# Kernel optimization log

Hardware: AMD Instinct MI355X
Metric: run time of the kernel (lower is better)

The kernel has to match this reference:

```python
import jax, jax.numpy as jnp
import numpy as np

IN_F = 256
LAYERS = [256, 256, 256, 256]   # layer_sizeList
DIMS = [IN_F] + LAYERS          # per-layer (in, out) = (DIMS[i], DIMS[i+1])
NUM_L = len(LAYERS)             # 4 dynamic layers (3 hidden + final identity)
CASE_IN = 64
CASE_H = 256
W_SIZE = IN_F * LAYERS[0]       # 65536, uniform across layers here
C, N = 64, 2048


def setup_inputs() -> dict:
    key = jax.random.key(0)
    k = jax.random.split(key, 8)
    x = jax.random.normal(k[0], (N, IN_F), jnp.float32)
    o = jax.random.normal(k[1], (C, CASE_IN), jnp.float32)
    # caseNN hidden layer (Linear + SiLU)
    Wc = jax.random.normal(k[2], (CASE_IN, CASE_H), jnp.float32) / np.sqrt(CASE_IN).astype(np.float32)
    bc = jnp.zeros((CASE_H,), jnp.float32)
    # final heads (identity activation): one weight head + one bias head per domain layer
    head_scale = np.float32(1.0 / (np.sqrt(CASE_H) * np.sqrt(IN_F)))
    Ww = jax.random.normal(k[3], (NUM_L, CASE_H, W_SIZE), jnp.float32) * head_scale
    bw = jnp.zeros((NUM_L, W_SIZE), jnp.float32)
    Wb = jax.random.normal(k[4], (NUM_L, CASE_H, LAYERS[0]), jnp.float32) * head_scale
    bb = jnp.zeros((NUM_L, LAYERS[0]), jnp.float32)
    return {"x": x, "o": o, "Wc": Wc, "bc": bc, "Ww": Ww, "bw": bw, "Wb": Wb, "bb": bb}


def reference(x, o, Wc, bc, Ww, bw, Wb, bb):
    # ---- caseNN (hypernetwork): generate per-case weights/biases ----
    h = jax.nn.silu(o @ Wc + bc)                     # [C, H]
    w = jnp.einsum('ch,lhd->lcd', h, Ww) + bw[:, None, :]   # [L, C, in*out]
    b = jnp.einsum('ch,lhd->lcd', h, Wb) + bb[:, None, :]   # [L, C, out]
    c = o.shape[0]

    # ---- domain net: per-case dynamic FC layers with skip connections ----
    # layer 0: broadcast shared x over cases
    W0 = w[0].reshape(c, DIMS[0], DIMS[1])
    y = jax.nn.silu(jnp.einsum('ni,cio->cno', x, W0) + b[0][:, None, :])  # [C, N, 256]
    x_skip = y  # skip_connections and i==0
    for i in range(1, NUM_L - 1):
        Wi = w[i].reshape(c, DIMS[i], DIMS[i + 1])
        y2 = jax.nn.silu(jnp.einsum('cni,cio->cno', y, Wi) + b[i][:, None, :])
        if i % 2 == 0:
            y2, x_skip = y2 + x_skip, y2
        y = y2
    # final layer: identity activation
    Wf = w[NUM_L - 1].reshape(c, DIMS[NUM_L - 1], DIMS[NUM_L])
    out = jnp.einsum('cni,cio->cno', y, Wf) + b[NUM_L - 1][:, None, :]
    return out.reshape(-1, out.shape[-1])  # [C*N, out]
```

## Files before the change

### kernel.cpp

```cpp
#include <hip/hip_runtime.h>


typedef __bf16 bf16;
typedef __bf16 bf16x4 __attribute__((ext_vector_type(4)));
typedef __bf16 bf16x8 __attribute__((ext_vector_type(8)));
typedef _Float16 f16;
typedef _Float16 f16x8 __attribute__((ext_vector_type(8)));
typedef float  f32x4  __attribute__((ext_vector_type(4)));
typedef unsigned short u16x8 __attribute__((ext_vector_type(8)));

#define AS1 __attribute__((address_space(1)))
#define AS3 __attribute__((address_space(3)))

__device__ __forceinline__ void gl2lds16(const void* g, void* l) {
  __builtin_amdgcn_global_load_lds((const AS1 unsigned int*)g,
                                   (AS3 unsigned int*)l, 16, 0, 0);
}

__device__ __forceinline__ float silu_f(float v) {
  return v / (1.0f + __expf(-v));
}

__global__ void k_hyper(const float* __restrict__ o, const float* __restrict__ Wc,
                        const float* __restrict__ bc, float* __restrict__ ht,
                        f16* __restrict__ hb16) {
  __shared__ float os[64];
  int c = blockIdx.x;
  int j = threadIdx.x;
  if (j < 64) os[j] = o[c * 64 + j];
  __syncthreads();
  float a = bc[j];
#pragma unroll
  for (int i = 0; i < 64; ++i) a = fmaf(os[i], Wc[i * 256 + j], a);
  float h = silu_f(a);
  ht[j * 64 + c] = h;
  hb16[c * 256 + j] = (f16)h;
}

__global__ void k_xcast(const float* __restrict__ x, bf16* __restrict__ xb) {
  int i = (blockIdx.x * 256 + threadIdx.x) * 4;
  float4 v = *(const float4*)(x + i);
  bf16x4 r = { (bf16)v.x, (bf16)v.y, (bf16)v.z, (bf16)v.w };
  *(bf16x4*)(xb + i) = r;
}

__global__ __launch_bounds__(512, 1) void k_genw(
    const float* __restrict__ Ww, const float* __restrict__ bw,
    const f16* __restrict__ hb16, bf16* __restrict__ wnat) {
  __shared__ __attribute__((aligned(16))) char Hs[32768];
  __shared__ __attribute__((aligned(16))) char Wslot[3][32768];
  int l = blockIdx.x >> 8;
  int d0 = (blockIdx.x & 255) * 256;
  const float* Wwl = Ww + (size_t)l * 16777216;
  int tid = threadIdx.x, lane = tid & 63, wid = tid >> 6;

  for (int q = tid; q < 2048; q += 512) {
    int c = q >> 5, g = q & 31;
    f16x8 v = *(const f16x8*)(hb16 + c * 256 + g * 8);
    *(f16x8*)(Hs + c * 512 + ((g ^ (c & 7)) << 4)) = v;
  }
  __syncthreads();

  auto STAGE = [&](int s, int t) {
#pragma unroll
    for (int ii = 0; ii < 4; ++ii) {
      int row = wid * 4 + ii;
      gl2lds16(Wwl + (size_t)(t * 32 + row) * 65536 + d0 + lane * 4,
               &Wslot[s][row * 1024]);
    }
  };

  f32x4 acc[4][2] = {};
  STAGE(0, 0);
  STAGE(1, 1);
#pragma unroll
  for (int kk = 0; kk < 8; ++kk) {
    if (kk < 6) STAGE((kk + 2) % 3, kk + 2);
    if (kk < 6)       asm volatile("s_waitcnt vmcnt(8)" ::: "memory");
    else if (kk == 6) asm volatile("s_waitcnt vmcnt(4)" ::: "memory");
    else              asm volatile("s_waitcnt vmcnt(0)" ::: "memory");
    __builtin_amdgcn_s_barrier();
    __builtin_amdgcn_sched_barrier(0);

    f16x8 af[4];
    int kc = kk * 4 + (lane >> 4);
#pragma unroll
    for (int mf = 0; mf < 4; ++mf) {
      int c = mf * 16 + (lane & 15);
      af[mf] = *(const f16x8*)(Hs + c * 512 + ((kc ^ (c & 7)) << 4));
    }
    const float* Ws = (const float*)&Wslot[kk % 3][0];
    f16x8 bfrag[2];
#pragma unroll
    for (int nf = 0; nf < 2; ++nf) {
      int n = wid * 32 + nf * 16 + (lane & 15);
#pragma unroll
      for (int j = 0; j < 8; ++j)
        bfrag[nf][j] = (f16)Ws[((lane >> 4) * 8 + j) * 256 + n];
    }
    asm volatile("s_waitcnt lgkmcnt(0)" ::: "memory");
    __builtin_amdgcn_sched_barrier(0);
    __builtin_amdgcn_s_barrier();
#pragma unroll
    for (int mf = 0; mf < 4; ++mf)
#pragma unroll
      for (int nf = 0; nf < 2; ++nf)
        acc[mf][nf] = __builtin_amdgcn_mfma_f32_16x16x32_f16(
            af[mf], bfrag[nf], acc[mf][nf], 0, 0, 0);
  }

#pragma unroll
  for (int nf = 0; nf < 2; ++nf) {
    int d = d0 + wid * 32 + nf * 16 + (lane & 15);
    float bv = bw[(size_t)l * 65536 + d];
#pragma unroll
    for (int mf = 0; mf < 4; ++mf) {
      int cb = mf * 16 + (lane >> 4) * 4;
#pragma unroll
      for (int r = 0; r < 4; ++r)
        wnat[(size_t)(l * 64 + cb + r) * 65536 + d] = (bf16)(acc[mf][nf][r] + bv);
    }
  }
}

__global__ void k_genb(const float* __restrict__ Wb, const float* __restrict__ bb,
                       const float* __restrict__ ht, float* __restrict__ bias) {
  __shared__ float red[4][256];
  int l = blockIdx.x >> 6;
  int c = blockIdx.x & 63;
  int q = threadIdx.x >> 8;
  int oo = threadIdx.x & 255;
  const float* wp = Wb + (size_t)l * 65536 + oo;
  float a = 0.f;
#pragma unroll 4
  for (int hh = q * 64; hh < q * 64 + 64; ++hh)
    a = fmaf(ht[hh * 64 + c], wp[hh * 256], a);
  red[q][oo] = a;
  __syncthreads();
  if (q == 0)
    bias[(size_t)(l * 64 + c) * 256 + oo] =
        red[0][oo] + red[1][oo] + red[2][oo] + red[3][oo] + bb[l * 256 + oo];
}

__global__ void k_tw(const unsigned short* __restrict__ w,
                     unsigned short* __restrict__ wt) {
  __shared__ __attribute__((aligned(16))) unsigned short T[64][64];
  int b = blockIdx.x;
  int lc = b >> 4, tile = b & 15;
  int i0 = (tile >> 2) << 6, o0 = (tile & 3) << 6;
  const unsigned short* src = w + (size_t)lc * 65536;
  unsigned short* dst = wt + (size_t)lc * 65536;
  int t = threadIdx.x;
  for (int q = t; q < 512; q += 256) {
    int r = q >> 3, cc = q & 7;
    u16x8 v = *(const u16x8*)(src + (size_t)(i0 + r) * 256 + o0 + cc * 8);
    *(u16x8*)&T[r][(cc ^ ((r >> 3) & 7)) * 8] = v;
  }
  __syncthreads();
  for (int q = t; q < 512; q += 256) {
    int r = q >> 3, cc = q & 7;
    u16x8 v;
#pragma unroll
    for (int e = 0; e < 8; ++e) {
      int il = cc * 8 + e;
      v[e] = T[il][((((r >> 3) ^ (il >> 3)) & 7) << 3) + (r & 7)];
    }
    *(u16x8*)(dst + (size_t)(o0 + r) * 256 + i0 + cc * 8) = v;
  }
}

template <int LAYER>
__global__ __launch_bounds__(256, 3) void k_gemm(
    const bf16* __restrict__ A_base, const bf16* __restrict__ WT,
    const float* __restrict__ BIAS, bf16* __restrict__ Yout,
    const bf16* __restrict__ Skip, float* __restrict__ Fout) {
  __shared__ __attribute__((aligned(16))) bf16 As[3][128 * 32];
  __shared__ __attribute__((aligned(16))) bf16 Bs[3][128 * 32];
  int bx = blockIdx.x;
  bx = (bx & 7) * 256 + (bx >> 3);
  int c  = bx >> 5;
  int tl = bx & 31;
  int m0 = (tl & 15) << 7;
  int n0 = (tl >> 4) << 7;
  int tid = threadIdx.x;
  int lane = tid & 63, wid = tid >> 6;
  int wm = wid >> 1, wn = wid & 1;

  const bf16* Ab = (LAYER == 0) ? A_base : (A_base + (size_t)c * 2048 * 256);
  const bf16* Bb = WT + (size_t)c * 65536;

  int qb = (wid << 7) + lane;
  int q2 = qb + 64;

  auto STAGE = [&](int slot, int t) {
    int k0 = t * 32;
    char* lA = (char*)&As[slot][0] + (wid << 11);
    char* lB = (char*)&Bs[slot][0] + (wid << 11);
    gl2lds16((const char*)(Ab + (size_t)(m0 + (qb >> 2)) * 256 + k0) + (qb & 3) * 16, lA);
    gl2lds16((const char*)(Ab + (size_t)(m0 + (q2 >> 2)) * 256 + k0) + (q2 & 3) * 16, lA + 1024);
    gl2lds16((const char*)(Bb + (size_t)(n0 + (qb >> 2)) * 256 + k0) + (qb & 3) * 16, lB);
    gl2lds16((const char*)(Bb + (size_t)(n0 + (q2 >> 2)) * 256 + k0) + (q2 & 3) * 16, lB + 1024);
  };

  f32x4 acc[4][4] = {};
  STAGE(0, 0);
  STAGE(1, 1);
#pragma unroll
  for (int kk = 0; kk < 8; ++kk) {
    if (kk < 6) STAGE((kk + 2) % 3, kk + 2);
    if (kk < 6)       asm volatile("s_waitcnt vmcnt(8)" ::: "memory");
    else if (kk == 6) asm volatile("s_waitcnt vmcnt(4)" ::: "memory");
    else              asm volatile("s_waitcnt vmcnt(0)" ::: "memory");
    __builtin_amdgcn_s_barrier();
    __builtin_amdgcn_sched_barrier(0);

    const bf16* Asl = &As[kk % 3][0];
    const bf16* Bsl = &Bs[kk % 3][0];
    bf16x8 af[4], bfr[4];
    int krow = (lane >> 4) * 8;
#pragma unroll
    for (int i = 0; i < 4; ++i) {
      af[i]  = *(const bf16x8*)&Asl[(wm * 64 + i * 16 + (lane & 15)) * 32 + krow];
      bfr[i] = *(const bf16x8*)&Bsl[(wn * 64 + i * 16 + (lane & 15)) * 32 + krow];
    }
    asm volatile("s_waitcnt lgkmcnt(0)" ::: "memory");
    __builtin_amdgcn_sched_barrier(0);
    __builtin_amdgcn_s_barrier();
#pragma unroll
    for (int i = 0; i < 4; ++i)
#pragma unroll
      for (int j = 0; j < 4; ++j)
        acc[i][j] = __builtin_amdgcn_mfma_f32_16x16x32_bf16(af[i], bfr[j],
                                                            acc[i][j], 0, 0, 0);
  }

  const float* bp = BIAS + c * 256;
#pragma unroll
  for (int i = 0; i < 4; ++i) {
    int row = m0 + wm * 64 + i * 16 + (lane >> 4) * 4;
#pragma unroll
    for (int j = 0; j < 4; ++j) {
      int col = n0 + wn * 64 + j * 16 + (lane & 15);
      float bv = bp[col];
#pragma unroll
      for (int r = 0; r < 4; ++r) {
        float v = acc[i][j][r] + bv;
        size_t idx = ((size_t)c * 2048 + (row + r)) * 256 + col;
        if (LAYER < 3) {
          float s = silu_f(v);
          if (LAYER == 2) s += (float)Skip[idx];
          Yout[idx] = (bf16)s;
        } else {
          Fout[idx] = v;
        }
      }
    }
  }
}

extern "C" void kernel_launch(void* const* d_in, const int* in_sizes, int n_in,
                              void* d_out, int out_size, void* d_ws, size_t ws_size,
                              hipStream_t stream) {
  const float* x  = (const float*)d_in[0];
  const float* o  = (const float*)d_in[1];
  const float* Wc = (const float*)d_in[2];
  const float* bc = (const float*)d_in[3];
  const float* Ww = (const float*)d_in[4];
  const float* bw = (const float*)d_in[5];
  const float* Wb = (const float*)d_in[6];
  const float* bb = (const float*)d_in[7];
  float* out = (float*)d_out;
  char* ws = (char*)d_ws;

  if (ws_size < 102072320ULL) return;
  bf16*  wt   = (bf16*)(ws);
  bf16*  buf0 = (bf16*)(ws + 33554432);
  float* bias = (float*)(ws + 100663296);
  float* ht   = (float*)(ws + 100925440);
  bf16*  xb   = (bf16*)(ws + 100990976);
  f16*   hb16 = (f16*)(ws + 102039552);
  bf16*  buf1 = (bf16*)(out);
  bf16*  wnat = (bf16*)((char*)out + 67108864);

  k_hyper<<<64, 256, 0, stream>>>(o, Wc, bc, ht, hb16);
  k_xcast<<<512, 256, 0, stream>>>(x, xb);
  k_genw<<<1024, 512, 0, stream>>>(Ww, bw, hb16, wnat);
  k_genb<<<256, 1024, 0, stream>>>(Wb, bb, ht, bias);
  k_tw<<<4096, 256, 0, stream>>>((const unsigned short*)wnat, (unsigned short*)wt);

  k_gemm<0><<<2048, 256, 0, stream>>>(xb,   wt,               bias,             buf0, nullptr, nullptr);
  k_gemm<1><<<2048, 256, 0, stream>>>(buf0, wt + 1 * 4194304, bias + 1 * 16384, buf1, nullptr, nullptr);
  k_gemm<2><<<2048, 256, 0, stream>>>(buf1, wt + 2 * 4194304, bias + 2 * 16384, buf0, buf0,    nullptr);
  k_gemm<3><<<2048, 256, 0, stream>>>(buf0, wt + 3 * 4194304, bias + 3 * 16384, nullptr, nullptr, out);
}
```

Before: 579.7 us.

## Widen GEMM tile to full 256 output columns with 8 waves and swizzled LDS

New measurement: 584.5 us. Within noise of the previous version (+0.8%).

```diff
diff --git a/kernel.cpp b/kernel.cpp
--- a/kernel.cpp
+++ b/kernel.cpp
@@ -170,68 +170,74 @@
 }
 
 template <int LAYER>
-__global__ __launch_bounds__(256, 3) void k_gemm(
+__global__ __launch_bounds__(512, 2) void k_gemm(
     const bf16* __restrict__ A_base, const bf16* __restrict__ WT,
     const float* __restrict__ BIAS, bf16* __restrict__ Yout,
     const bf16* __restrict__ Skip, float* __restrict__ Fout) {
   __shared__ __attribute__((aligned(16))) bf16 As[3][128 * 32];
-  __shared__ __attribute__((aligned(16))) bf16 Bs[3][128 * 32];
+  __shared__ __attribute__((aligned(16))) bf16 Bs[3][256 * 32];
   int bx = blockIdx.x;
-  bx = (bx & 7) * 256 + (bx >> 3);
-  int c  = bx >> 5;
-  int tl = bx & 31;
-  int m0 = (tl & 15) << 7;
-  int n0 = (tl >> 4) << 7;
+  bx = (bx & 7) * 128 + (bx >> 3);
+  int c  = bx >> 4;
+  int m0 = (bx & 15) << 7;
   int tid = threadIdx.x;
   int lane = tid & 63, wid = tid >> 6;
-  int wm = wid >> 1, wn = wid & 1;
+  int wm = wid >> 2, wn = wid & 3;
 
   const bf16* Ab = (LAYER == 0) ? A_base : (A_base + (size_t)c * 2048 * 256);
   const bf16* Bb = WT + (size_t)c * 65536;
 
-  int qb = (wid << 7) + lane;
-  int q2 = qb + 64;
+  int q  = (wid << 6) + lane;
+  int row_q = q >> 2, kc_q = q & 3;
+  int skA = kc_q ^ ((row_q >> 1) & 3);
+  int q2 = q + 512;
+  int row_q2 = q2 >> 2;
+  int skB2 = kc_q ^ ((row_q2 >> 1) & 3);
 
   auto STAGE = [&](int slot, int t) {
     int k0 = t * 32;
-    char* lA = (char*)&As[slot][0] + (wid << 11);
-    char* lB = (char*)&Bs[slot][0] + (wid << 11);
-    gl2lds16((const char*)(Ab + (size_t)(m0 + (qb >> 2)) * 256 + k0) + (qb & 3) * 16, lA);
-    gl2lds16((const char*)(Ab + (size_t)(m0 + (q2 >> 2)) * 256 + k0) + (q2 & 3) * 16, lA + 1024);
-    gl2lds16((const char*)(Bb + (size_t)(n0 + (qb >> 2)) * 256 + k0) + (qb & 3) * 16, lB);
-    gl2lds16((const char*)(Bb + (size_t)(n0 + (q2 >> 2)) * 256 + k0) + (q2 & 3) * 16, lB + 1024);
+    gl2lds16(Ab + (size_t)(m0 + row_q) * 256 + k0 + skA * 8,
+             (char*)&As[slot][0] + (wid << 10));
+    gl2lds16(Bb + (size_t)row_q * 256 + k0 + skA * 8,
+             (char*)&Bs[slot][0] + (wid << 10));
+    gl2lds16(Bb + (size_t)row_q2 * 256 + k0 + skB2 * 8,
+             (char*)&Bs[slot][0] + 8192 + (wid << 10));
   };
 
   f32x4 acc[4][4] = {};
   STAGE(0, 0);
   STAGE(1, 1);
+  int kcw = lane >> 4;
 #pragma unroll
   for (int kk = 0; kk < 8; ++kk) {
     if (kk < 6) STAGE((kk + 2) % 3, kk + 2);
-    if (kk < 6)       asm volatile("s_waitcnt vmcnt(8)" ::: "memory");
-    else if (kk == 6) asm volatile("s_waitcnt vmcnt(4)" ::: "memory");
+    if (kk < 6)       asm volatile("s_waitcnt vmcnt(6)" ::: "memory");
+    else if (kk == 6) asm volatile("s_waitcnt vmcnt(3)" ::: "memory");
     else              asm volatile("s_waitcnt vmcnt(0)" ::: "memory");
     __builtin_amdgcn_s_barrier();
     __builtin_amdgcn_sched_barrier(0);
 
-    const bf16* Asl = &As[kk % 3][0];
-    const bf16* Bsl = &Bs[kk % 3][0];
+    const char* Asl = (const char*)&As[kk % 3][0];
+    const char* Bsl = (const char*)&Bs[kk % 3][0];
     bf16x8 af[4], bfr[4];
-    int krow = (lane >> 4) * 8;
 #pragma unroll
     for (int i = 0; i < 4; ++i) {
-      af[i]  = *(const bf16x8*)&Asl[(wm * 64 + i * 16 + (lane & 15)) * 32 + krow];
-      bfr[i] = *(const bf16x8*)&Bsl[(wn * 64 + i * 16 + (lane & 15)) * 32 + krow];
+      int ra = wm * 64 + i * 16 + (lane & 15);
+      af[i] = *(const bf16x8*)(Asl + ra * 64 + ((kcw ^ ((ra >> 1) & 3)) << 4));
+      int rb = wn * 64 + i * 16 + (lane & 15);
+      bfr[i] = *(const bf16x8*)(Bsl + rb * 64 + ((kcw ^ ((rb >> 1) & 3)) << 4));
     }
     asm volatile("s_waitcnt lgkmcnt(0)" ::: "memory");
     __builtin_amdgcn_sched_barrier(0);
     __builtin_amdgcn_s_barrier();
+    __builtin_amdgcn_s_setprio(1);
 #pragma unroll
     for (int i = 0; i < 4; ++i)
 #pragma unroll
       for (int j = 0; j < 4; ++j)
         acc[i][j] = __builtin_amdgcn_mfma_f32_16x16x32_bf16(af[i], bfr[j],
                                                             acc[i][j], 0, 0, 0);
+    __builtin_amdgcn_s_setprio(0);
   }
 
   const float* bp = BIAS + c * 256;
@@ -240,7 +246,7 @@
     int row = m0 + wm * 64 + i * 16 + (lane >> 4) * 4;
 #pragma unroll
     for (int j = 0; j < 4; ++j) {
-      int col = n0 + wn * 64 + j * 16 + (lane & 15);
+      int col = wn * 64 + j * 16 + (lane & 15);
       float bv = bp[col];
 #pragma unroll
       for (int r = 0; r < 4; ++r) {
@@ -288,8 +294,8 @@
   k_genb<<<256, 1024, 0, stream>>>(Wb, bb, ht, bias);
   k_tw<<<4096, 256, 0, stream>>>((const unsigned short*)wnat, (unsigned short*)wt);
 
-  k_gemm<0><<<2048, 256, 0, stream>>>(xb,   wt,               bias,             buf0, nullptr, nullptr);
-  k_gemm<1><<<2048, 256, 0, stream>>>(buf0, wt + 1 * 4194304, bias + 1 * 16384, buf1, nullptr, nullptr);
-  k_gemm<2><<<2048, 256, 0, stream>>>(buf1, wt + 2 * 4194304, bias + 2 * 16384, buf0, buf0,    nullptr);
-  k_gemm<3><<<2048, 256, 0, stream>>>(buf0, wt + 3 * 4194304, bias + 3 * 16384, nullptr, nullptr, out);
-}
+  k_gemm<0><<<1024, 512, 0, stream>>>(xb,   wt,               bias,             buf0, nullptr, nullptr);
+  k_gemm<1><<<1024, 512, 0, stream>>>(buf0, wt + 1 * 4194304, bias + 1 * 16384, buf1, nullptr, nullptr);
+  k_gemm<2><<<1024, 512, 0, stream>>>(buf1, wt + 2 * 4194304, bias + 2 * 16384, buf0, buf0,    nullptr);
+  k_gemm<3><<<1024, 512, 0, stream>>>(buf0, wt + 3 * 4194304, bias + 3 * 16384, nullptr, nullptr, out);
+}
```
